# Optimization experiments

Measured on AMD Instinct MI355X. Metric: run time of the kernel, lower is better.

Reference implementation:

```python
import math
import jax, jax.numpy as jnp
import numpy as np

B, N, M = 8, 2048, 1024
INPUT_SIZE = 512
HEAD_DIM = 64
NUM_HEADS = 6
ATTN_SIZE = HEAD_DIM * NUM_HEADS
MAX_CLASSES = 512


def setup_inputs() -> dict:
    key = jax.random.key(0)
    k1, k2, k3, k4, k5, k6, k7 = jax.random.split(key, 7)
    bound = 1.0 / math.sqrt(INPUT_SIZE)
    return {
        "train_embeddings": jax.random.normal(k1, (B, N, INPUT_SIZE), jnp.float32),
        "test_embeddings": jax.random.normal(k2, (B, M, INPUT_SIZE), jnp.float32),
        "targets": jax.random.randint(k3, (B, N), 0, MAX_CLASSES),
        # torch nn.Linear weights, stored as [in, out] for direct matmul
        "Wq": jax.random.uniform(k4, (INPUT_SIZE, ATTN_SIZE), jnp.float32, -bound, bound),
        "bq": jax.random.uniform(k5, (ATTN_SIZE,), jnp.float32, -bound, bound),
        "Wk": jax.random.uniform(k6, (INPUT_SIZE, ATTN_SIZE), jnp.float32, -bound, bound),
        "bk": jax.random.uniform(k7, (ATTN_SIZE,), jnp.float32, -bound, bound),
    }


def reference(train_embeddings, test_embeddings, targets, Wq, bq, Wk, bk):
    b, m, _ = test_embeddings.shape
    # projections -> [B, S, H, D]
    q_bmhd = (test_embeddings @ Wq + bq).reshape(b, m, NUM_HEADS, HEAD_DIM)
    k_bnhd = (train_embeddings @ Wk + bk).reshape(b, -1, NUM_HEADS, HEAD_DIM)
    scale = 1.0 / math.sqrt(HEAD_DIM)  # SDPA default scale
    # attention scores [B, H, M, N]
    scores = jnp.einsum("bmhd,bnhd->bhmn", q_bmhd, k_bnhd) * scale
    attn = jax.nn.softmax(scores, axis=-1)
    # one-hot train targets [B, N, C]; chunk-folding in the torch code is a
    # memory trick — mathematically it is just attn @ one_hot per head
    onehot_bnc = jax.nn.one_hot(targets, MAX_CLASSES, dtype=q_bmhd.dtype)
    out_bhmc = jnp.einsum("bhmn,bnc->bhmc", attn, onehot_bnc)
    out_bmc = out_bhmc.mean(axis=1)          # mean over heads
    out_mbc = out_bmc.transpose(1, 0, 2)      # [M, B, C]
    return jnp.log(jnp.clip(out_mbc, 1e-05) + 3e-05)
```

## Files before the change

kernel.cpp:

```cpp
#include <hip/hip_runtime.h>
#include <hip/hip_bf16.h>

#define BQ 8
#define NN 2048
#define MM 1024
#define EE 512
#define NH 6
#define AA 384
#define CC 512

#define KROW_B (AA * 2)
#define TILE_B (16 * KROW_B)
#define STILE_B (32 * KROW_B)
#define WROW_B (EE * 2)
#define WTILE_B (16 * WROW_B)

#define QSCALE 0.1803368801111204f

typedef __bf16 bf16x8 __attribute__((ext_vector_type(8)));
typedef float  f32x4  __attribute__((ext_vector_type(4)));
using bf16 = __hip_bfloat16;

static __device__ __forceinline__ f32x4 mfma16(bf16x8 a, bf16x8 b, f32x4 c) {
  return __builtin_amdgcn_mfma_f32_16x16x32_bf16(a, b, c, 0, 0, 0);
}

typedef __attribute__((address_space(1))) const void gconst_void;
typedef __attribute__((address_space(3))) void lds_void_t;
static __device__ __forceinline__ void ld_lds16(const void* g, void* l) {
  __builtin_amdgcn_global_load_lds((gconst_void*)g, (lds_void_t*)l, 16, 0, 0);
}

static __device__ __forceinline__ unsigned enc_fp8(float f) {
  unsigned b = __float_as_uint(f) + 0x00080000u;
  int e = (int)((b >> 23) & 0xFF) - 120;
  if (e <= 0) return 0u;
  if (e >= 16) return 0x7Eu;
  return ((unsigned)e << 3) | ((b >> 20) & 7u);
}
static __device__ __forceinline__ float dec_fp8(unsigned u) {
  unsigned e = (u >> 3) & 0xFu;
  if (e == 0) return 0.f;
  return __uint_as_float(((e + 120u) << 23) | ((u & 7u) << 20));
}
static __device__ __forceinline__ unsigned pk4(float a, float b, float c, float d) {
#if __has_builtin(__builtin_amdgcn_cvt_pk_fp8_f32)
  int v = __builtin_amdgcn_cvt_pk_fp8_f32(a, b, 0, false);
  v = __builtin_amdgcn_cvt_pk_fp8_f32(c, d, v, true);
  return (unsigned)v;
#else
  return enc_fp8(a) | (enc_fp8(b) << 8) | (enc_fp8(c) << 16) | (enc_fp8(d) << 24);
#endif
}
static __device__ __forceinline__ unsigned pk2(float a, float b) {
#if __has_builtin(__builtin_amdgcn_cvt_pk_fp8_f32)
  return (unsigned)__builtin_amdgcn_cvt_pk_fp8_f32(a, b, 0, false);
#else
  return enc_fp8(a) | (enc_fp8(b) << 8);
#endif
}
template <int SEL>
static __device__ __forceinline__ float up8(unsigned d) {
#if __has_builtin(__builtin_amdgcn_cvt_f32_fp8)
  return __builtin_amdgcn_cvt_f32_fp8((int)d, SEL);
#else
  return dec_fp8((d >> (SEL * 8)) & 0xFFu);
#endif
}

__global__ __launch_bounds__(512) void prep_kernel(
    const float* __restrict__ Wq, const float* __restrict__ Wk,
    bf16* __restrict__ WqT, bf16* __restrict__ WkT,
    const int* __restrict__ targets, int* __restrict__ cnts, int* __restrict__ idxP)
{
  __shared__ float t[64][65];
  __shared__ int cnt[CC], pos[CC];
  int bid = blockIdx.x, tid = threadIdx.x;
  if (bid < 96) {
    if (tid >= 256) { __syncthreads(); return; }
    int id = bid;
    const float* W = (id < 48) ? Wq : Wk;
    bf16* WT = (id < 48) ? WqT : WkT;
    if (id >= 48) id -= 48;
    int kb = (id / 6) * 64, nb = (id % 6) * 64;
    int lr = tid >> 4, lc = (tid & 15) * 4;
    #pragma unroll
    for (int p = 0; p < 4; p++) {
      int k = lr + p * 16;
      float4 v = *reinterpret_cast<const float4*>(W + (size_t)(kb + k) * AA + nb + lc);
      t[k][lc] = v.x; t[k][lc + 1] = v.y; t[k][lc + 2] = v.z; t[k][lc + 3] = v.w;
    }
    __syncthreads();
    #pragma unroll
    for (int p = 0; p < 4; p++) {
      int n = lr + p * 16;
      bf16* dst = WT + (size_t)(nb + n) * EE + kb + lc;
      dst[0] = __float2bfloat16(t[lc][n]);
      dst[1] = __float2bfloat16(t[lc + 1][n]);
      dst[2] = __float2bfloat16(t[lc + 2][n]);
      dst[3] = __float2bfloat16(t[lc + 3][n]);
    }
    return;
  }
  int b = bid - 96;
  cnt[tid] = 0;
  pos[tid] = 0;
  int4 sent = make_int4(NN, NN, NN, NN);
  int4* prow = reinterpret_cast<int4*>(idxP + ((size_t)b * CC + tid) * 32);
  #pragma unroll
  for (int i = 0; i < 8; i++) prow[i] = sent;
  __syncthreads();
  int tv[4];
  #pragma unroll
  for (int i = 0; i < 4; i++) {
    tv[i] = targets[b * NN + tid * 4 + i];
    atomicAdd(&cnt[tv[i]], 1);
  }
  __syncthreads();
  cnts[b * CC + tid] = cnt[tid];
  __syncthreads();
  #pragma unroll
  for (int i = 0; i < 4; i++) {
    int p = atomicAdd(&pos[tv[i]], 1);
    if (p < 32) idxP[((size_t)b * CC + tv[i]) * 32 + p] = tid * 4 + i;
  }
}

__global__ __launch_bounds__(256, 3) void proj_kernel(
    const float* __restrict__ test, const float* __restrict__ train,
    const bf16* __restrict__ WqT, const bf16* __restrict__ WkT,
    const float* __restrict__ bq, const float* __restrict__ bk,
    bf16* __restrict__ Qb, bf16* __restrict__ Kb)
{
  __shared__ char wbuf[3][WTILE_B];
  int tid = threadIdx.x, wid = tid >> 6, lane = tid & 63;
  int bid = blockIdx.x;
  int sub = bid & 1, unit = bid >> 1;
  const float* A; const bf16* WT; const float* bias; bf16* C; float scale; int m0;
  if (unit < 128) { A = test;  WT = WqT; bias = bq; C = Qb; scale = QSCALE; m0 = unit * 64; }
  else            { A = train; WT = WkT; bias = bk; C = Kb; scale = 1.0f;   m0 = (unit - 128) * 64; }
  m0 += wid * 16;
  int row = lane & 15, hi = lane >> 4;

  bf16x8 af[16];
  const float* arow = A + (size_t)(m0 + row) * EE + hi * 8;
  #pragma unroll
  for (int ks = 0; ks < 16; ks++) {
    float4 u = *reinterpret_cast<const float4*>(arow + ks * 32);
    float4 v = *reinterpret_cast<const float4*>(arow + ks * 32 + 4);
    bf16x8 f;
    f[0] = (__bf16)u.x; f[1] = (__bf16)u.y; f[2] = (__bf16)u.z; f[3] = (__bf16)u.w;
    f[4] = (__bf16)v.x; f[5] = (__bf16)v.y; f[6] = (__bf16)v.z; f[7] = (__bf16)v.w;
    af[ks] = f;
  }

  int ldso[4], srco[4];
  #pragma unroll
  for (int i = 0; i < 4; i++) {
    int off = tid * 16 + i * 4096;
    int rw = off >> 10, c = off & 1023;
    ldso[i] = off;
    srco[i] = rw * WROW_B + (c ^ ((rw & 7) << 4));
  }
  const char* wgbase = (const char*)WT + (size_t)sub * 12 * WTILE_B;
  int sw = (row & 7) << 4;

  auto stage = [&](int t, int buf) {
    const char* src = wgbase + (size_t)t * WTILE_B;
    #pragma unroll
    for (int i = 0; i < 4; i++) ld_lds16(src + srco[i], wbuf[buf] + ldso[i]);
  };
  auto compute = [&](int buf, int t) {
    const char* wb = wbuf[buf] + row * WROW_B;
    f32x4 acc0 = {0.f, 0.f, 0.f, 0.f}, acc1 = {0.f, 0.f, 0.f, 0.f};
    #pragma unroll
    for (int ks = 0; ks < 16; ks += 2) {
      bf16x8 w0 = *reinterpret_cast<const bf16x8*>(wb + ((hi * 16 + ks * 64) ^ sw));
      bf16x8 w1 = *reinterpret_cast<const bf16x8*>(wb + ((hi * 16 + (ks + 1) * 64) ^ sw));
      acc0 = mfma16(af[ks], w0, acc0);
      acc1 = mfma16(af[ks + 1], w1, acc1);
    }
    f32x4 acc = acc0 + acc1;
    int ocol = (sub * 12 + t) * 16 + row;
    float bv = bias[ocol];
    #pragma unroll
    for (int j = 0; j < 4; j++)
      C[(size_t)(m0 + hi * 4 + j) * AA + ocol] = __float2bfloat16((acc[j] + bv) * scale);
  };

  stage(0, 0);
  stage(1, 1);
  asm volatile("s_waitcnt vmcnt(4)" ::: "memory");
  __builtin_amdgcn_s_barrier();
  __builtin_amdgcn_sched_barrier(0);
  stage(2, 2);
  compute(0, 0);

  int cur = 1, stg = 0;
  #pragma unroll 1
  for (int t = 1; t < 11; t++) {
    asm volatile("s_waitcnt vmcnt(8)" ::: "memory");
    __builtin_amdgcn_s_barrier();
    __builtin_amdgcn_sched_barrier(0);
    if (t < 10) stage(t + 2, stg);
    compute(cur, t);
    cur = cur + 1 < 3 ? cur + 1 : 0;
    stg = stg + 1 < 3 ? stg + 1 : 0;
  }
  asm volatile("s_waitcnt vmcnt(4)" ::: "memory");
  __builtin_amdgcn_s_barrier();
  __builtin_amdgcn_sched_barrier(0);
  compute(cur, 11);
}

__global__ __launch_bounds__(256, 2) void spass_kernel(
    const bf16* __restrict__ Qb, const bf16* __restrict__ Kb, char* __restrict__ Wh)
{
  __shared__ char kbuf[2][STILE_B];
  int id = blockIdx.x;
  int b = id & 7, r = id >> 3, mt = r & 7, nc = r >> 3;
  int tid = threadIdx.x, wid = tid >> 6, lane = tid & 63;
  int m0 = mt * 128 + wid * 32, n0 = nc * 256;
  int row = lane & 15, hi = lane >> 4;

  bf16x8 qf[2][12];
  #pragma unroll
  for (int s = 0; s < 2; s++) {
    const bf16* qrow = Qb + ((size_t)(b * MM + m0 + s * 16 + row)) * AA + hi * 8;
    #pragma unroll
    for (int ks = 0; ks < 12; ks++) qf[s][ks] = *reinterpret_cast<const bf16x8*>(qrow + ks * 32);
  }

  int ldso[6], srco[6];
  #pragma unroll
  for (int i = 0; i < 6; i++) {
    int off = tid * 16 + i * 4096;
    int rw = off / KROW_B, c = off - rw * KROW_B;
    ldso[i] = off;
    srco[i] = rw * KROW_B + (c ^ ((rw & 7) << 4));
  }
  const char* kgbase = (const char*)(Kb + ((size_t)(b * NN + n0)) * AA);

  int sw = (row & 7) << 4;
  int rbase = row * KROW_B;
  int x0 = rbase + ((hi * 16) ^ sw);
  int x1 = rbase + (((hi * 16) + 64) ^ sw);

  auto stage = [&](int t, int buf) {
    const char* src = kgbase + (size_t)t * STILE_B;
    #pragma unroll
    for (int i = 0; i < 6; i++) ld_lds16(src + srco[i], kbuf[buf] + ldso[i]);
  };
  auto compute = [&](int buf, int st) {
    #pragma unroll
    for (int sub = 0; sub < 2; sub++) {
      const char* kb = kbuf[buf] + sub * TILE_B;
      float w[2][NH][4];
      __builtin_amdgcn_s_setprio(1);
      #pragma unroll
      for (int h = 0; h < NH; h++) {
        bf16x8 k0 = *reinterpret_cast<const bf16x8*>(kb + h * 128 + x0);
        bf16x8 k1 = *reinterpret_cast<const bf16x8*>(kb + h * 128 + x1);
        f32x4 a0 = {0.f, 0.f, 0.f, 0.f}, a1 = {0.f, 0.f, 0.f, 0.f};
        a0 = mfma16(qf[0][2 * h], k0, a0);
        a1 = mfma16(qf[1][2 * h], k0, a1);
        a0 = mfma16(qf[0][2 * h + 1], k1, a0);
        a1 = mfma16(qf[1][2 * h + 1], k1, a1);
        #pragma unroll
        for (int j = 0; j < 4; j++) {
          w[0][h][j] = __builtin_amdgcn_exp2f(a0[j]);
          w[1][h][j] = __builtin_amdgcn_exp2f(a1[j]);
        }
      }
      __builtin_amdgcn_s_setprio(0);
      int n = n0 + (st * 2 + sub) * 16 + row;
      #pragma unroll
      for (int s = 0; s < 2; s++)
        #pragma unroll
        for (int j = 0; j < 4; j++) {
          unsigned d0 = pk4(w[s][0][j], w[s][1][j], w[s][2][j], w[s][3][j]);
          unsigned d1 = pk2(w[s][4][j], w[s][5][j]);
          int m = m0 + s * 16 + hi * 4 + j;
          *reinterpret_cast<uint2*>(Wh + (((size_t)(b * MM + m)) * NN + n) * 8) = make_uint2(d0, d1);
        }
    }
  };

  stage(0, 0);
  asm volatile("s_waitcnt vmcnt(0)" ::: "memory");
  __builtin_amdgcn_s_barrier();
  __builtin_amdgcn_sched_barrier(0);
  stage(1, 1);
  compute(0, 0);

  #pragma unroll 1
  for (int i = 1; i < 8; i++) {
    asm volatile("s_waitcnt vmcnt(16)" ::: "memory");
    __builtin_amdgcn_s_barrier();
    __builtin_amdgcn_sched_barrier(0);
    if (i < 7) stage(i + 1, (i + 1) & 1);
    compute(i & 1, i);
  }
}

__global__ __launch_bounds__(512) void gather_kernel(
    const char* __restrict__ Wh, const int* __restrict__ cnts,
    const int* __restrict__ idxP, float* __restrict__ out)
{
  __shared__ uint2 wl[2][2050];
  __shared__ float wred[8][12];
  __shared__ float rzs[12];
  int id = blockIdx.x;
  int b = id & 7, mt = id >> 3;
  int m0 = mt * 2;
  int tid = threadIdx.x, wid = tid >> 6, lane = tid & 63;

  #pragma unroll
  for (int m = 0; m < 2; m++) {
    const uint4* src = (const uint4*)(Wh + ((size_t)(b * MM + m0 + m) * NN) * 8);
    uint4* dst = (uint4*)&wl[m][0];
    #pragma unroll 2
    for (int i = tid; i < NN / 2; i += 512) dst[i] = src[i];
  }
  if (tid < 2) wl[tid][2048] = make_uint2(0u, 0u);
  __syncthreads();

  int c = tid;
  int kc = cnts[b * CC + c];
  const int* ip = idxP + ((size_t)b * CC + c) * 32;
  float B[2][NH];
  #pragma unroll
  for (int m = 0; m < 2; m++)
    #pragma unroll
    for (int h = 0; h < NH; h++) B[m][h] = 0.f;

  int kcp = (kc + 3) & ~3;
  #pragma unroll 1
  for (int i = 0; i < kcp; i += 4) {
    int4 ia = *reinterpret_cast<const int4*>(ip + i);
    int idxs4[4] = {ia.x, ia.y, ia.z, ia.w};
    #pragma unroll
    for (int e = 0; e < 4; e++) {
      int idx = idxs4[e];
      #pragma unroll
      for (int m = 0; m < 2; m++) {
        uint2 v = wl[m][idx];
        B[m][0] += up8<0>(v.x); B[m][1] += up8<1>(v.x);
        B[m][2] += up8<2>(v.x); B[m][3] += up8<3>(v.x);
        B[m][4] += up8<0>(v.y); B[m][5] += up8<1>(v.y);
      }
    }
  }

  #pragma unroll
  for (int m = 0; m < 2; m++)
    #pragma unroll
    for (int h = 0; h < NH; h++) {
      float t = B[m][h];
      t += __shfl_xor(t, 1);  t += __shfl_xor(t, 2);  t += __shfl_xor(t, 4);
      t += __shfl_xor(t, 8);  t += __shfl_xor(t, 16); t += __shfl_xor(t, 32);
      if (lane == 0) wred[wid][m * NH + h] = t;
    }
  __syncthreads();
  if (tid < 12) {
    float z = 0.f;
    #pragma unroll
    for (int w = 0; w < 8; w++) z += wred[w][tid];
    rzs[tid] = 1.0f / (6.0f * z);
  }
  __syncthreads();

  #pragma unroll
  for (int m = 0; m < 2; m++) {
    float v = 0.f;
    #pragma unroll
    for (int h = 0; h < NH; h++) v += B[m][h] * rzs[m * NH + h];
    out[((size_t)(m0 + m) * BQ + b) * CC + c] = __logf(fmaxf(v, 1e-5f) + 3e-5f);
  }
}

extern "C" void kernel_launch(void* const* d_in, const int* in_sizes, int n_in,
                              void* d_out, int out_size, void* d_ws, size_t ws_size,
                              hipStream_t stream) {
  const float* train = (const float*)d_in[0];
  const float* test  = (const float*)d_in[1];
  const int*   tgt   = (const int*)d_in[2];
  const float* Wq    = (const float*)d_in[3];
  const float* bq    = (const float*)d_in[4];
  const float* Wk    = (const float*)d_in[5];
  const float* bk    = (const float*)d_in[6];
  float* out = (float*)d_out;

  char* ws = (char*)d_ws;
  bf16*  WqT  = (bf16*)(ws);
  bf16*  WkT  = (bf16*)(ws + 393216);
  bf16*  Qb   = (bf16*)(ws + 786432);
  bf16*  Kb   = (bf16*)(ws + 7077888);
  char*  Wh   = (char*)(ws + 19660800);
  int*   cnts = (int*)(ws + 153878528);
  int*   idxP = (int*)(ws + 153894912);

  prep_kernel<<<104, 512, 0, stream>>>(Wq, Wk, WqT, WkT, tgt, cnts, idxP);
  proj_kernel<<<768, 256, 0, stream>>>(test, train, WqT, WkT, bq, bk, Qb, Kb);
  spass_kernel<<<512, 256, 0, stream>>>(Qb, Kb, Wh);
  gather_kernel<<<4096, 512, 0, stream>>>(Wh, cnts, idxP, out);
}
```

Before: 109.2 us.

## Gather directly from global memory with four query rows per block

The gather kernel no longer stages two full query rows of fp8 attention weights into LDS. It now issues direct global loads of 8-byte entries, with padding indices redirected to a zeroed scratch word, and it processes four query rows per block, which halves the grid. The aim is to remove the LDS fill and barrier and to reuse each index load across more rows. The cost is scattered, uncoalesced global reads that depend on L2 and cache hit rates, plus higher register use per thread.

```diff
diff --git a/kernel.cpp b/kernel.cpp
--- a/kernel.cpp
+++ b/kernel.cpp
@@ -71,7 +71,8 @@
 __global__ __launch_bounds__(512) void prep_kernel(
     const float* __restrict__ Wq, const float* __restrict__ Wk,
     bf16* __restrict__ WqT, bf16* __restrict__ WkT,
-    const int* __restrict__ targets, int* __restrict__ cnts, int* __restrict__ idxP)
+    const int* __restrict__ targets, int* __restrict__ cnts, int* __restrict__ idxP,
+    char* __restrict__ zbuf)
 {
   __shared__ float t[64][65];
   __shared__ int cnt[CC], pos[CC];
@@ -103,6 +104,7 @@
     return;
   }
   int b = bid - 96;
+  if (b == 0 && tid == 0) *reinterpret_cast<unsigned long long*>(zbuf) = 0ull;
   cnt[tid] = 0;
   pos[tid] = 0;
   int4 sent = make_int4(NN, NN, NN, NN);
@@ -305,32 +307,24 @@
 
 __global__ __launch_bounds__(512) void gather_kernel(
     const char* __restrict__ Wh, const int* __restrict__ cnts,
-    const int* __restrict__ idxP, float* __restrict__ out)
+    const int* __restrict__ idxP, const char* __restrict__ zbuf,
+    float* __restrict__ out)
 {
-  __shared__ uint2 wl[2][2050];
-  __shared__ float wred[8][12];
-  __shared__ float rzs[12];
+  __shared__ float wred[8][24];
+  __shared__ float rzs[24];
   int id = blockIdx.x;
   int b = id & 7, mt = id >> 3;
-  int m0 = mt * 2;
+  int m0 = mt * 4;
   int tid = threadIdx.x, wid = tid >> 6, lane = tid & 63;
-
-  #pragma unroll
-  for (int m = 0; m < 2; m++) {
-    const uint4* src = (const uint4*)(Wh + ((size_t)(b * MM + m0 + m) * NN) * 8);
-    uint4* dst = (uint4*)&wl[m][0];
-    #pragma unroll 2
-    for (int i = tid; i < NN / 2; i += 512) dst[i] = src[i];
-  }
-  if (tid < 2) wl[tid][2048] = make_uint2(0u, 0u);
-  __syncthreads();
 
   int c = tid;
   int kc = cnts[b * CC + c];
   const int* ip = idxP + ((size_t)b * CC + c) * 32;
-  float B[2][NH];
-  #pragma unroll
-  for (int m = 0; m < 2; m++)
+  const char* rbase = Wh + ((size_t)(b * MM + m0)) * (NN * 8);
+
+  float B[4][NH];
+  #pragma unroll
+  for (int m = 0; m < 4; m++)
     #pragma unroll
     for (int h = 0; h < NH; h++) B[m][h] = 0.f;
 
@@ -338,22 +332,30 @@
   #pragma unroll 1
   for (int i = 0; i < kcp; i += 4) {
     int4 ia = *reinterpret_cast<const int4*>(ip + i);
-    int idxs4[4] = {ia.x, ia.y, ia.z, ia.w};
+    int e4[4] = {ia.x, ia.y, ia.z, ia.w};
+    uint2 v[4][4];
     #pragma unroll
     for (int e = 0; e < 4; e++) {
-      int idx = idxs4[e];
+      int idx = e4[e];
       #pragma unroll
-      for (int m = 0; m < 2; m++) {
-        uint2 v = wl[m][idx];
-        B[m][0] += up8<0>(v.x); B[m][1] += up8<1>(v.x);
-        B[m][2] += up8<2>(v.x); B[m][3] += up8<3>(v.x);
-        B[m][4] += up8<0>(v.y); B[m][5] += up8<1>(v.y);
+      for (int m = 0; m < 4; m++) {
+        const char* p = (idx < NN) ? (rbase + (size_t)m * (NN * 8) + (size_t)idx * 8) : zbuf;
+        v[e][m] = *reinterpret_cast<const uint2*>(p);
       }
     }
-  }
-
-  #pragma unroll
-  for (int m = 0; m < 2; m++)
+    #pragma unroll
+    for (int e = 0; e < 4; e++)
+      #pragma unroll
+      for (int m = 0; m < 4; m++) {
+        uint2 u = v[e][m];
+        B[m][0] += up8<0>(u.x); B[m][1] += up8<1>(u.x);
+        B[m][2] += up8<2>(u.x); B[m][3] += up8<3>(u.x);
+        B[m][4] += up8<0>(u.y); B[m][5] += up8<1>(u.y);
+      }
+  }
+
+  #pragma unroll
+  for (int m = 0; m < 4; m++)
     #pragma unroll
     for (int h = 0; h < NH; h++) {
       float t = B[m][h];
@@ -362,7 +364,7 @@
       if (lane == 0) wred[wid][m * NH + h] = t;
     }
   __syncthreads();
-  if (tid < 12) {
+  if (tid < 24) {
     float z = 0.f;
     #pragma unroll
     for (int w = 0; w < 8; w++) z += wred[w][tid];
@@ -371,7 +373,7 @@
   __syncthreads();
 
   #pragma unroll
-  for (int m = 0; m < 2; m++) {
+  for (int m = 0; m < 4; m++) {
     float v = 0.f;
     #pragma unroll
     for (int h = 0; h < NH; h++) v += B[m][h] * rzs[m * NH + h];
@@ -399,9 +401,10 @@
   char*  Wh   = (char*)(ws + 19660800);
   int*   cnts = (int*)(ws + 153878528);
   int*   idxP = (int*)(ws + 153894912);
-
-  prep_kernel<<<104, 512, 0, stream>>>(Wq, Wk, WqT, WkT, tgt, cnts, idxP);
+  char*  zbuf = (char*)(ws + 154419200);
+
+  prep_kernel<<<104, 512, 0, stream>>>(Wq, Wk, WqT, WkT, tgt, cnts, idxP, zbuf);
   proj_kernel<<<768, 256, 0, stream>>>(test, train, WqT, WkT, bq, bk, Qb, Kb);
   spass_kernel<<<512, 256, 0, stream>>>(Qb, Kb, Wh);
-  gather_kernel<<<4096, 512, 0, stream>>>(Wh, cnts, idxP, out);
-}
+  gather_kernel<<<2048, 512, 0, stream>>>(Wh, cnts, idxP, zbuf, out);
+}
```

Result: slower. 136.5 us (+25.0%).
